# Performance work log

Measured on AMD Instinct MI355X. Metric: run time of the kernel, lower is better.

Reference implementation:

```python
import jax, jax.numpy as jnp
import numpy as np

NUM_ITER = 3  # self.num_iter


def setup_inputs() -> dict:
    key = jax.random.key(0)
    k1, k2, k3 = jax.random.split(key, 3)
    B, N, D = 8, 8192, 512          # batch, num_particles, dimension
    P, G, GS = 4, 512, 16           # num projs, groups per proj, group size
    x = jax.random.normal(k1, (B, N, D), dtype=jnp.float32)
    # per-proj feature projection (stand-in for proj.get_delta_x); small scale for stability
    W = jax.random.normal(k2, (P, D, D), dtype=jnp.float32) * 0.02
    groups = jax.random.randint(k3, (P, G, GS), 0, N, dtype=jnp.int32)
    return {"x": x, "W": W, "groups": groups}


def reference(x, W, groups):
    # x: [B, N, D]; W: [P, D, D]; groups: [P, G, GS] indices into N
    B, N, D = x.shape
    P = W.shape[0]
    upd = x
    for ite in range(NUM_ITER):
        scale = 1.0 / (ite + 1)  # ite-dependence of get_delta_x
        delta = jnp.zeros_like(upd)
        for i in range(P):
            g = groups[i]                      # [G, GS]
            gx = upd[:, g, :]                  # gather -> [B, G, GS, D]
            dx = scale * jnp.einsum('bgsd,de->bgse', gx, W[i])
            # scatter-add deltas back onto particle axis (overlaps accumulate)
            delta = delta.at[:, g.reshape(-1), :].add(dx.reshape(B, -1, D))
        upd = upd + delta
    return upd
```

## Files before the change

kernel.cpp:

```cpp
#include <hip/hip_runtime.h>
#include <stdint.h>

#define NROW 8192
#define DDIM 512
#define BB   8
#define PP   4
#define MTOT (BB*NROW)

typedef __attribute__((ext_vector_type(8))) short short8;
typedef __attribute__((ext_vector_type(4))) float floatx4;
typedef __attribute__((ext_vector_type(4))) unsigned int uintx4;

__device__ inline float bf2f(unsigned short h) { return __uint_as_float(((unsigned)h) << 16); }
__device__ inline unsigned short f2bf_rn(float f) {
    return (unsigned short)((__float_as_uint(f) + 0x8000u) >> 16);
}
__device__ inline unsigned pack_bf16(float a, float b) {
    unsigned ua = __float_as_uint(a) + 0x8000u;
    unsigned ub = __float_as_uint(b) + 0x8000u;
    return __builtin_amdgcn_perm(ub, ua, 0x07060302u);
}

template <typename T> __device__ inline float loadF(const T* p);
template <> __device__ inline float loadF<float>(const float* p) { return *p; }
template <> __device__ inline float loadF<unsigned short>(const unsigned short* p) { return bf2f(*p); }
template <typename T> __device__ inline void storeF(T* p, float f);
template <> __device__ inline void storeF<float>(float* p, float f) { *p = f; }
template <> __device__ inline void storeF<unsigned short>(unsigned short* p, float f) { *p = f2bf_rn(f); }

__global__ void hist_kernel(const int* __restrict__ groups, float* __restrict__ cnt) {
    int t = blockIdx.x * 256 + threadIdx.x;
    int i = t >> 13;
    atomicAdd(&cnt[i * NROW + groups[t]], 1.0f);
}

__global__ void transpose_w(const float* __restrict__ W, unsigned short* __restrict__ Wsw) {
    int u = blockIdx.x * 256 + threadIdx.x;
    int i    = u >> 15;
    int kb   = (u >> 11) & 15;
    int gt   = (u >> 6) & 31;
    int lane = u & 63;
    int n  = gt * 16 + (lane & 15);
    int k0 = kb * 32 + (lane >> 4) * 8;
    const float* wp = W + i * 262144 + k0 * 512 + n;
    unsigned hp[4];
    #pragma unroll
    for (int j = 0; j < 4; ++j)
        hp[j] = pack_bf16(wp[(2*j) * 512], wp[(2*j+1) * 512]);
    uintx4 w = {hp[0], hp[1], hp[2], hp[3]};
    *(uintx4*)(Wsw + (size_t)u * 8) = w;
}

template <typename SrcT, typename DstT>
__global__ __launch_bounds__(256, 2)
void gemm_round(const SrcT* __restrict__ src, const unsigned short* __restrict__ Wsw,
                const float* __restrict__ cnt, DstT* __restrict__ dst, float scale)
{
    __shared__ __align__(16) unsigned short sA[2][2048];
    __shared__ __align__(16) float sE[PP][16][64];

    const int t    = threadIdx.x;
    const int wave = t >> 6;
    const int lane = t & 63;
    const int m0   = blockIdx.x * 64;
    const int nb   = blockIdx.y;

    float cs[4][4];
    #pragma unroll
    for (int a = 0; a < 4; ++a)
        #pragma unroll
        for (int q = 0; q < 4; ++q)
            cs[a][q] = cnt[wave * NROW + ((m0 + a*16 + (lane >> 4)*4 + q) & (NROW - 1))];

    const int srow = ((t >> 6) << 4) | (t & 15);
    const int scol = ((t >> 4) & 3) * 8;
    const SrcT* sp = src + (size_t)(m0 + srow) * DDIM + scol;
    unsigned short* sAw0 = &sA[0][t * 8];
    unsigned short* sAw1 = &sA[1][t * 8];

    const unsigned short* bp = Wsw + ((size_t)(wave * 16) * 32 + nb * 4) * 512 + lane * 8;

    floatx4 acc[4][4] = {};
    short8 Bc[2][4];

    #pragma unroll
    for (int b = 0; b < 4; ++b)
        Bc[0][b] = *(const short8*)(bp + b * 512);
    if constexpr (sizeof(SrcT) == 4) {
        floatx4 v0 = *(const floatx4*)(sp);
        floatx4 v1 = *(const floatx4*)(sp + 4);
        uintx4 w = { pack_bf16(v0[0], v0[1]), pack_bf16(v0[2], v0[3]),
                     pack_bf16(v1[0], v1[1]), pack_bf16(v1[2], v1[3]) };
        *(uintx4*)sAw0 = w;
    } else {
        *(uintx4*)sAw0 = *(const uintx4*)sp;
    }
    __syncthreads();

    #pragma unroll
    for (int kb = 0; kb < 16; ++kb) {
        const int cur = kb & 1;
        unsigned short* sAwn = cur ? sAw0 : sAw1;

        floatx4 v0, v1; uintx4 vr;
        if (kb < 15) {
            if constexpr (sizeof(SrcT) == 4) {
                v0 = *(const floatx4*)(sp + (kb + 1) * 32);
                v1 = *(const floatx4*)(sp + (kb + 1) * 32 + 4);
            } else {
                vr = *(const uintx4*)(sp + (kb + 1) * 32);
            }
            #pragma unroll
            for (int b = 0; b < 4; ++b)
                Bc[cur ^ 1][b] = *(const short8*)(bp + (size_t)(kb + 1) * 16384 + b * 512);
        }

        short8 af[4];
        #pragma unroll
        for (int a = 0; a < 4; ++a)
            af[a] = *(const short8*)&sA[cur][(a * 64 + lane) * 8];

        #pragma unroll
        for (int a = 0; a < 4; ++a)
            #pragma unroll
            for (int b = 0; b < 4; ++b)
                acc[a][b] = __builtin_amdgcn_mfma_f32_16x16x32_bf16(af[a], Bc[cur][b], acc[a][b], 0, 0, 0);

        if (kb < 15) {
            if constexpr (sizeof(SrcT) == 4) {
                uintx4 w = { pack_bf16(v0[0], v0[1]), pack_bf16(v0[2], v0[3]),
                             pack_bf16(v1[0], v1[1]), pack_bf16(v1[2], v1[3]) };
                *(uintx4*)sAwn = w;
            } else {
                *(uintx4*)sAwn = vr;
            }
        }
        __syncthreads();
    }

    #pragma unroll
    for (int a = 0; a < 4; ++a) {
        #pragma unroll
        for (int b = 0; b < 4; ++b)
            #pragma unroll
            for (int q = 0; q < 4; ++q)
                sE[wave][(lane >> 4) * 4 + q][b * 16 + (lane & 15)] = acc[a][b][q] * cs[a][q];
        __syncthreads();
        #pragma unroll
        for (int e = 0; e < 4; ++e) {
            const int r = wave * 4 + e;
            const size_t m = (size_t)(m0 + a * 16 + r);
            const size_t n = (size_t)nb * 64 + lane;
            const float sum = sE[0][r][lane] + sE[1][r][lane] + sE[2][r][lane] + sE[3][r][lane];
            storeF(dst + m * DDIM + n, loadF(src + m * DDIM + n) + scale * sum);
        }
        if (a < 3) __syncthreads();
    }
}

extern "C" void kernel_launch(void* const* d_in, const int* in_sizes, int n_in,
                              void* d_out, int out_size, void* d_ws, size_t ws_size,
                              hipStream_t stream) {
    const float* x      = (const float*)d_in[0];
    const float* W      = (const float*)d_in[1];
    const int*   groups = (const int*)d_in[2];
    float* out = (float*)d_out;

    char* ws = (char*)d_ws;
    float*          cnt = (float*)ws;
    unsigned short* Wsw = (unsigned short*)(ws + 131072);
    unsigned short* U   = (unsigned short*)(ws + 131072 + 2097152);

    hipMemsetAsync(cnt, 0, PP * NROW * sizeof(float), stream);
    hist_kernel<<<32768 / 256, 256, 0, stream>>>(groups, cnt);
    transpose_w<<<131072 / 256, 256, 0, stream>>>(W, Wsw);

    dim3 grid(MTOT / 64, DDIM / 64);
    gemm_round<float, float><<<grid, 256, 0, stream>>>(x, Wsw, cnt, out, 1.0f);
    gemm_round<float, unsigned short><<<grid, 256, 0, stream>>>(out, Wsw, cnt, U, 0.5f);
    gemm_round<unsigned short, float><<<grid, 256, 0, stream>>>(U, Wsw, cnt, out, 1.0f / 3.0f);
}
```

Before: 862.8 us.

## Deepen GEMM pipeline with two-stage k-steps, swap grid order, pad epilogue LDS

Restructures the gemm_round main loop to process two k-blocks per barrier, using a register prefetch two stages ahead and a lighter LDS-only barrier. This halves the number of block syncs. The grid is transposed so the N-blocks sharing one 64-row M-tile are launched together, which should improve L2 reuse of the source rows. It also aliases the epilogue buffer onto the A-tile shared memory and pads its rows to 65 to avoid bank conflicts. The cost is higher register pressure from the prefetch buffers, and relying on a custom barrier that only waits on lgkmcnt.

```diff
diff --git a/kernel.cpp b/kernel.cpp
--- a/kernel.cpp
+++ b/kernel.cpp
@@ -19,6 +19,11 @@
     unsigned ua = __float_as_uint(a) + 0x8000u;
     unsigned ub = __float_as_uint(b) + 0x8000u;
     return __builtin_amdgcn_perm(ub, ua, 0x07060302u);
+}
+__device__ inline uintx4 packA(const floatx4& v0, const floatx4& v1) {
+    uintx4 w = { pack_bf16(v0[0], v0[1]), pack_bf16(v0[2], v0[3]),
+                 pack_bf16(v1[0], v1[1]), pack_bf16(v1[2], v1[3]) };
+    return w;
 }
 
 template <typename T> __device__ inline float loadF(const T* p);
@@ -27,6 +32,13 @@
 template <typename T> __device__ inline void storeF(T* p, float f);
 template <> __device__ inline void storeF<float>(float* p, float f) { *p = f; }
 template <> __device__ inline void storeF<unsigned short>(unsigned short* p, float f) { *p = f2bf_rn(f); }
+
+__device__ inline void block_sync_lds() {
+    __builtin_amdgcn_sched_barrier(0);
+    asm volatile("s_waitcnt lgkmcnt(0)" ::: "memory");
+    __builtin_amdgcn_s_barrier();
+    __builtin_amdgcn_sched_barrier(0);
+}
 
 __global__ void hist_kernel(const int* __restrict__ groups, float* __restrict__ cnt) {
     int t = blockIdx.x * 256 + threadIdx.x;
@@ -56,102 +68,139 @@
 void gemm_round(const SrcT* __restrict__ src, const unsigned short* __restrict__ Wsw,
                 const float* __restrict__ cnt, DstT* __restrict__ dst, float scale)
 {
-    __shared__ __align__(16) unsigned short sA[2][2048];
-    __shared__ __align__(16) float sE[PP][16][64];
+    __shared__ __align__(16) unsigned char smem[16768];
+    unsigned short* sA = (unsigned short*)smem;
+    float*          sE = (float*)smem;
 
     const int t    = threadIdx.x;
     const int wave = t >> 6;
     const int lane = t & 63;
-    const int m0   = blockIdx.x * 64;
-    const int nb   = blockIdx.y;
-
-    float cs[4][4];
-    #pragma unroll
-    for (int a = 0; a < 4; ++a)
-        #pragma unroll
-        for (int q = 0; q < 4; ++q)
-            cs[a][q] = cnt[wave * NROW + ((m0 + a*16 + (lane >> 4)*4 + q) & (NROW - 1))];
+    const int nb   = blockIdx.x;
+    const int m0   = blockIdx.y * 64;
 
     const int srow = ((t >> 6) << 4) | (t & 15);
     const int scol = ((t >> 4) & 3) * 8;
     const SrcT* sp = src + (size_t)(m0 + srow) * DDIM + scol;
-    unsigned short* sAw0 = &sA[0][t * 8];
-    unsigned short* sAw1 = &sA[1][t * 8];
+    unsigned short* sAw = sA + t * 8;
 
     const unsigned short* bp = Wsw + ((size_t)(wave * 16) * 32 + nb * 4) * 512 + lane * 8;
 
     floatx4 acc[4][4] = {};
-    short8 Bc[2][4];
-
+    short8 Bf[2][4];
+    floatx4 pf[2][2];
+    uintx4  pb[2];
+
+    #pragma unroll
+    for (int s = 0; s < 2; ++s) {
+        if constexpr (sizeof(SrcT) == 4) {
+            floatx4 v0 = *(const floatx4*)(sp + s * 32);
+            floatx4 v1 = *(const floatx4*)(sp + s * 32 + 4);
+            *(uintx4*)(sAw + s * 2048) = packA(v0, v1);
+        } else {
+            *(uintx4*)(sAw + s * 2048) = *(const uintx4*)(sp + s * 32);
+        }
+    }
+    #pragma unroll
+    for (int s = 0; s < 2; ++s) {
+        if constexpr (sizeof(SrcT) == 4) {
+            pf[s][0] = *(const floatx4*)(sp + (2 + s) * 32);
+            pf[s][1] = *(const floatx4*)(sp + (2 + s) * 32 + 4);
+        } else {
+            pb[s] = *(const uintx4*)(sp + (2 + s) * 32);
+        }
+    }
     #pragma unroll
     for (int b = 0; b < 4; ++b)
-        Bc[0][b] = *(const short8*)(bp + b * 512);
-    if constexpr (sizeof(SrcT) == 4) {
-        floatx4 v0 = *(const floatx4*)(sp);
-        floatx4 v1 = *(const floatx4*)(sp + 4);
-        uintx4 w = { pack_bf16(v0[0], v0[1]), pack_bf16(v0[2], v0[3]),
-                     pack_bf16(v1[0], v1[1]), pack_bf16(v1[2], v1[3]) };
-        *(uintx4*)sAw0 = w;
-    } else {
-        *(uintx4*)sAw0 = *(const uintx4*)sp;
-    }
-    __syncthreads();
-
-    #pragma unroll
-    for (int kb = 0; kb < 16; ++kb) {
-        const int cur = kb & 1;
-        unsigned short* sAwn = cur ? sAw0 : sAw1;
-
-        floatx4 v0, v1; uintx4 vr;
-        if (kb < 15) {
-            if constexpr (sizeof(SrcT) == 4) {
-                v0 = *(const floatx4*)(sp + (kb + 1) * 32);
-                v1 = *(const floatx4*)(sp + (kb + 1) * 32 + 4);
-            } else {
-                vr = *(const uintx4*)(sp + (kb + 1) * 32);
+        Bf[0][b] = *(const short8*)(bp + b * 512);
+    block_sync_lds();
+
+    #pragma unroll
+    for (int it = 0; it < 8; ++it) {
+        const int buf = it & 1;
+        const unsigned short* sAr = sA + buf * 4096;
+
+        #pragma unroll
+        for (int b = 0; b < 4; ++b)
+            Bf[1][b] = *(const short8*)(bp + (size_t)(2 * it + 1) * 16384 + b * 512);
+
+        {
+            short8 af[4];
+            #pragma unroll
+            for (int a = 0; a < 4; ++a)
+                af[a] = *(const short8*)(sAr + (a * 64 + lane) * 8);
+            #pragma unroll
+            for (int a = 0; a < 4; ++a)
+                #pragma unroll
+                for (int b = 0; b < 4; ++b)
+                    acc[a][b] = __builtin_amdgcn_mfma_f32_16x16x32_bf16(af[a], Bf[0][b], acc[a][b], 0, 0, 0);
+        }
+
+        if (it < 7) {
+            #pragma unroll
+            for (int b = 0; b < 4; ++b)
+                Bf[0][b] = *(const short8*)(bp + (size_t)(2 * it + 2) * 16384 + b * 512);
+        }
+
+        {
+            short8 af[4];
+            #pragma unroll
+            for (int a = 0; a < 4; ++a)
+                af[a] = *(const short8*)(sAr + 2048 + (a * 64 + lane) * 8);
+            #pragma unroll
+            for (int a = 0; a < 4; ++a)
+                #pragma unroll
+                for (int b = 0; b < 4; ++b)
+                    acc[a][b] = __builtin_amdgcn_mfma_f32_16x16x32_bf16(af[a], Bf[1][b], acc[a][b], 0, 0, 0);
+        }
+
+        if (it < 7) {
+            unsigned short* sAn = sA + (buf ^ 1) * 4096 + t * 8;
+            #pragma unroll
+            for (int s = 0; s < 2; ++s) {
+                if constexpr (sizeof(SrcT) == 4)
+                    *(uintx4*)(sAn + s * 2048) = packA(pf[s][0], pf[s][1]);
+                else
+                    *(uintx4*)(sAn + s * 2048) = pb[s];
             }
-            #pragma unroll
-            for (int b = 0; b < 4; ++b)
-                Bc[cur ^ 1][b] = *(const short8*)(bp + (size_t)(kb + 1) * 16384 + b * 512);
-        }
-
-        short8 af[4];
-        #pragma unroll
-        for (int a = 0; a < 4; ++a)
-            af[a] = *(const short8*)&sA[cur][(a * 64 + lane) * 8];
-
-        #pragma unroll
-        for (int a = 0; a < 4; ++a)
-            #pragma unroll
-            for (int b = 0; b < 4; ++b)
-                acc[a][b] = __builtin_amdgcn_mfma_f32_16x16x32_bf16(af[a], Bc[cur][b], acc[a][b], 0, 0, 0);
-
-        if (kb < 15) {
-            if constexpr (sizeof(SrcT) == 4) {
-                uintx4 w = { pack_bf16(v0[0], v0[1]), pack_bf16(v0[2], v0[3]),
-                             pack_bf16(v1[0], v1[1]), pack_bf16(v1[2], v1[3]) };
-                *(uintx4*)sAwn = w;
-            } else {
-                *(uintx4*)sAwn = vr;
+            if (it < 6) {
+                #pragma unroll
+                for (int s = 0; s < 2; ++s) {
+                    const int c = (2 * (it + 2) + s) * 32;
+                    if constexpr (sizeof(SrcT) == 4) {
+                        pf[s][0] = *(const floatx4*)(sp + c);
+                        pf[s][1] = *(const floatx4*)(sp + c + 4);
+                    } else {
+                        pb[s] = *(const uintx4*)(sp + c);
+                    }
+                }
             }
         }
-        __syncthreads();
-    }
+        block_sync_lds();
+    }
+
+    float cs[4][4];
+    #pragma unroll
+    for (int a = 0; a < 4; ++a)
+        #pragma unroll
+        for (int q = 0; q < 4; ++q)
+            cs[a][q] = cnt[wave * NROW + ((m0 + a * 16 + (lane >> 4) * 4 + q) & (NROW - 1))];
 
     #pragma unroll
     for (int a = 0; a < 4; ++a) {
+        float* se = sE + wave * 1040;
         #pragma unroll
         for (int b = 0; b < 4; ++b)
             #pragma unroll
             for (int q = 0; q < 4; ++q)
-                sE[wave][(lane >> 4) * 4 + q][b * 16 + (lane & 15)] = acc[a][b][q] * cs[a][q];
+                se[((lane >> 4) * 4 + q) * 65 + b * 16 + (lane & 15)] = acc[a][b][q] * cs[a][q];
         __syncthreads();
         #pragma unroll
         for (int e = 0; e < 4; ++e) {
             const int r = wave * 4 + e;
             const size_t m = (size_t)(m0 + a * 16 + r);
             const size_t n = (size_t)nb * 64 + lane;
-            const float sum = sE[0][r][lane] + sE[1][r][lane] + sE[2][r][lane] + sE[3][r][lane];
+            const float sum = sE[0 * 1040 + r * 65 + lane] + sE[1 * 1040 + r * 65 + lane]
+                            + sE[2 * 1040 + r * 65 + lane] + sE[3 * 1040 + r * 65 + lane];
             storeF(dst + m * DDIM + n, loadF(src + m * DDIM + n) + scale * sum);
         }
         if (a < 3) __syncthreads();
@@ -175,7 +224,7 @@
     hist_kernel<<<32768 / 256, 256, 0, stream>>>(groups, cnt);
     transpose_w<<<131072 / 256, 256, 0, stream>>>(W, Wsw);
 
-    dim3 grid(MTOT / 64, DDIM / 64);
+    dim3 grid(DDIM / 64, MTOT / 64);
     gemm_round<float, float><<<grid, 256, 0, stream>>>(x, Wsw, cnt, out, 1.0f);
     gemm_round<float, unsigned short><<<grid, 256, 0, stream>>>(out, Wsw, cnt, U, 0.5f);
     gemm_round<unsigned short, float><<<grid, 256, 0, stream>>>(U, Wsw, cnt, out, 1.0f / 3.0f);
```

Measured after the change: 776.1 us. 1.11x faster.

## Stage bf16 A tiles via global_load_lds with triple-buffered pipeline

Applied to the files above, without the earlier changes.

Inputs are now converted to bf16 up front in a separate kernel. Each round writes a bf16 copy of its output alongside (or instead of) fp32, so every GEMM reads the A operand as bf16. A tiles are loaded straight into LDS with global_load_lds in a three-buffer ring paced by explicit vmcnt waits. W fragments are prefetched four slots deep in registers. The grid is reordered so consecutive blocks share an M tile across N blocks, and the epilogue LDS is padded to avoid bank conflicts. The aim is to remove the register-staged conversion and the per-k-step full barriers, at the cost of an extra conversion pass and more writes of bf16 intermediates.

```diff
diff --git a/kernel.cpp b/kernel.cpp
--- a/kernel.cpp
+++ b/kernel.cpp
@@ -20,13 +20,28 @@
     unsigned ub = __float_as_uint(b) + 0x8000u;
     return __builtin_amdgcn_perm(ub, ua, 0x07060302u);
 }
+__device__ inline uintx4 packA(const floatx4& v0, const floatx4& v1) {
+    uintx4 w = { pack_bf16(v0[0], v0[1]), pack_bf16(v0[2], v0[3]),
+                 pack_bf16(v1[0], v1[1]), pack_bf16(v1[2], v1[3]) };
+    return w;
+}
 
 template <typename T> __device__ inline float loadF(const T* p);
 template <> __device__ inline float loadF<float>(const float* p) { return *p; }
 template <> __device__ inline float loadF<unsigned short>(const unsigned short* p) { return bf2f(*p); }
-template <typename T> __device__ inline void storeF(T* p, float f);
-template <> __device__ inline void storeF<float>(float* p, float f) { *p = f; }
-template <> __device__ inline void storeF<unsigned short>(unsigned short* p, float f) { *p = f2bf_rn(f); }
+
+__device__ inline void glds16(const void* g, void* l) {
+    __builtin_amdgcn_global_load_lds(
+        (const __attribute__((address_space(1))) void*)g,
+        (__attribute__((address_space(3))) void*)l, 16, 0, 0);
+}
+
+#define SYNC_VM(N) do {                                                 \
+    __builtin_amdgcn_sched_barrier(0);                                  \
+    asm volatile("s_waitcnt vmcnt(" #N ") lgkmcnt(0)" ::: "memory");    \
+    __builtin_amdgcn_s_barrier();                                       \
+    __builtin_amdgcn_sched_barrier(0);                                  \
+} while (0)
 
 __global__ void hist_kernel(const int* __restrict__ groups, float* __restrict__ cnt) {
     int t = blockIdx.x * 256 + threadIdx.x;
@@ -51,108 +66,116 @@
     *(uintx4*)(Wsw + (size_t)u * 8) = w;
 }
 
-template <typename SrcT, typename DstT>
+__global__ void cvt_bf16(const float* __restrict__ x, unsigned short* __restrict__ xb) {
+    size_t t = (size_t)blockIdx.x * 256 + threadIdx.x;
+    const floatx4* p = (const floatx4*)x + t * 2;
+    floatx4 v0 = p[0], v1 = p[1];
+    *(uintx4*)(xb + t * 8) = packA(v0, v1);
+}
+
+template <typename AddT, bool WF32, bool WBF16>
 __global__ __launch_bounds__(256, 2)
-void gemm_round(const SrcT* __restrict__ src, const unsigned short* __restrict__ Wsw,
-                const float* __restrict__ cnt, DstT* __restrict__ dst, float scale)
+void gemm_round(const unsigned short* __restrict__ srcA, const AddT* __restrict__ srcAdd,
+                const unsigned short* __restrict__ Wsw, const float* __restrict__ cnt,
+                float* __restrict__ dstF, unsigned short* __restrict__ dstB, float scale)
 {
-    __shared__ __align__(16) unsigned short sA[2][2048];
-    __shared__ __align__(16) float sE[PP][16][64];
+    __shared__ __align__(16) unsigned char smem[24576];
+    float* sE = (float*)smem;
 
     const int t    = threadIdx.x;
     const int wave = t >> 6;
     const int lane = t & 63;
-    const int m0   = blockIdx.x * 64;
-    const int nb   = blockIdx.y;
+    const int nb   = blockIdx.x;
+    const int m0   = blockIdx.y * 64;
+
+    const int srow = (wave << 4) | (lane & 15);
+    const int scol = ((lane >> 4) & 3) * 8;
+    const unsigned short* sp = srcA + (size_t)(m0 + srow) * DDIM + scol;
+
+    const unsigned short* bp = Wsw + ((size_t)(wave * 16) * 32 + nb * 4) * 512 + lane * 8;
+
+    floatx4 acc[4][4] = {};
+    short8 Bf[4][4];
+
+    auto stage = [&](int buf, int it2) {
+        #pragma unroll
+        for (int s = 0; s < 2; ++s)
+            glds16(sp + (2 * it2 + s) * 32, smem + (buf * 2 + s) * 4096 + wave * 1024);
+    };
+    auto loadB = [&](int slot, int s) {
+        #pragma unroll
+        for (int b = 0; b < 4; ++b)
+            Bf[slot][b] = *(const short8*)(bp + (size_t)s * 16384 + b * 512);
+    };
+
+    stage(0, 0);
+    stage(1, 1);
+    __builtin_amdgcn_sched_barrier(0);
+    loadB(0, 0); loadB(1, 1); loadB(2, 2);
+    SYNC_VM(14);
+
+    #pragma unroll
+    for (int it = 0; it < 8; ++it) {
+        const unsigned short* sAr = (const unsigned short*)(smem + (it % 3) * 8192);
+
+        short8 af[2][4];
+        #pragma unroll
+        for (int s = 0; s < 2; ++s)
+            #pragma unroll
+            for (int a = 0; a < 4; ++a)
+                af[s][a] = *(const short8*)(sAr + s * 2048 + (a * 64 + lane) * 8);
+
+        if (it < 6) stage((it + 2) % 3, it + 2);
+        __builtin_amdgcn_sched_barrier(0);
+        if (it < 7) loadB((2 * it + 3) & 3, 2 * it + 3);
+        __builtin_amdgcn_sched_barrier(0);
+
+        #pragma unroll
+        for (int a = 0; a < 4; ++a)
+            #pragma unroll
+            for (int b = 0; b < 4; ++b)
+                acc[a][b] = __builtin_amdgcn_mfma_f32_16x16x32_bf16(af[0][a], Bf[(2 * it) & 3][b], acc[a][b], 0, 0, 0);
+
+        if (it < 6) loadB((2 * it + 4) & 3, 2 * it + 4);
+        __builtin_amdgcn_sched_barrier(0);
+
+        #pragma unroll
+        for (int a = 0; a < 4; ++a)
+            #pragma unroll
+            for (int b = 0; b < 4; ++b)
+                acc[a][b] = __builtin_amdgcn_mfma_f32_16x16x32_bf16(af[1][a], Bf[(2 * it + 1) & 3][b], acc[a][b], 0, 0, 0);
+
+        if (it < 6)       SYNC_VM(10);
+        else if (it == 6) SYNC_VM(4);
+        else              SYNC_VM(0);
+    }
 
     float cs[4][4];
     #pragma unroll
     for (int a = 0; a < 4; ++a)
         #pragma unroll
         for (int q = 0; q < 4; ++q)
-            cs[a][q] = cnt[wave * NROW + ((m0 + a*16 + (lane >> 4)*4 + q) & (NROW - 1))];
-
-    const int srow = ((t >> 6) << 4) | (t & 15);
-    const int scol = ((t >> 4) & 3) * 8;
-    const SrcT* sp = src + (size_t)(m0 + srow) * DDIM + scol;
-    unsigned short* sAw0 = &sA[0][t * 8];
-    unsigned short* sAw1 = &sA[1][t * 8];
-
-    const unsigned short* bp = Wsw + ((size_t)(wave * 16) * 32 + nb * 4) * 512 + lane * 8;
-
-    floatx4 acc[4][4] = {};
-    short8 Bc[2][4];
-
-    #pragma unroll
-    for (int b = 0; b < 4; ++b)
-        Bc[0][b] = *(const short8*)(bp + b * 512);
-    if constexpr (sizeof(SrcT) == 4) {
-        floatx4 v0 = *(const floatx4*)(sp);
-        floatx4 v1 = *(const floatx4*)(sp + 4);
-        uintx4 w = { pack_bf16(v0[0], v0[1]), pack_bf16(v0[2], v0[3]),
-                     pack_bf16(v1[0], v1[1]), pack_bf16(v1[2], v1[3]) };
-        *(uintx4*)sAw0 = w;
-    } else {
-        *(uintx4*)sAw0 = *(const uintx4*)sp;
-    }
-    __syncthreads();
-
-    #pragma unroll
-    for (int kb = 0; kb < 16; ++kb) {
-        const int cur = kb & 1;
-        unsigned short* sAwn = cur ? sAw0 : sAw1;
-
-        floatx4 v0, v1; uintx4 vr;
-        if (kb < 15) {
-            if constexpr (sizeof(SrcT) == 4) {
-                v0 = *(const floatx4*)(sp + (kb + 1) * 32);
-                v1 = *(const floatx4*)(sp + (kb + 1) * 32 + 4);
-            } else {
-                vr = *(const uintx4*)(sp + (kb + 1) * 32);
-            }
-            #pragma unroll
-            for (int b = 0; b < 4; ++b)
-                Bc[cur ^ 1][b] = *(const short8*)(bp + (size_t)(kb + 1) * 16384 + b * 512);
-        }
-
-        short8 af[4];
-        #pragma unroll
-        for (int a = 0; a < 4; ++a)
-            af[a] = *(const short8*)&sA[cur][(a * 64 + lane) * 8];
-
-        #pragma unroll
-        for (int a = 0; a < 4; ++a)
-            #pragma unroll
-            for (int b = 0; b < 4; ++b)
-                acc[a][b] = __builtin_amdgcn_mfma_f32_16x16x32_bf16(af[a], Bc[cur][b], acc[a][b], 0, 0, 0);
-
-        if (kb < 15) {
-            if constexpr (sizeof(SrcT) == 4) {
-                uintx4 w = { pack_bf16(v0[0], v0[1]), pack_bf16(v0[2], v0[3]),
-                             pack_bf16(v1[0], v1[1]), pack_bf16(v1[2], v1[3]) };
-                *(uintx4*)sAwn = w;
-            } else {
-                *(uintx4*)sAwn = vr;
-            }
-        }
-        __syncthreads();
-    }
+            cs[a][q] = cnt[wave * NROW + ((m0 + a * 16 + (lane >> 4) * 4 + q) & (NROW - 1))];
 
     #pragma unroll
     for (int a = 0; a < 4; ++a) {
+        float* se = sE + wave * 1104;
         #pragma unroll
         for (int b = 0; b < 4; ++b)
             #pragma unroll
             for (int q = 0; q < 4; ++q)
-                sE[wave][(lane >> 4) * 4 + q][b * 16 + (lane & 15)] = acc[a][b][q] * cs[a][q];
+                se[((lane >> 4) * 4 + q) * 69 + b * 16 + (lane & 15)] = acc[a][b][q] * cs[a][q];
         __syncthreads();
         #pragma unroll
         for (int e = 0; e < 4; ++e) {
             const int r = wave * 4 + e;
             const size_t m = (size_t)(m0 + a * 16 + r);
             const size_t n = (size_t)nb * 64 + lane;
-            const float sum = sE[0][r][lane] + sE[1][r][lane] + sE[2][r][lane] + sE[3][r][lane];
-            storeF(dst + m * DDIM + n, loadF(src + m * DDIM + n) + scale * sum);
+            const float sum = sE[0 * 1104 + r * 69 + lane] + sE[1 * 1104 + r * 69 + lane]
+                            + sE[2 * 1104 + r * 69 + lane] + sE[3 * 1104 + r * 69 + lane];
+            const float f = loadF(srcAdd + m * DDIM + n) + scale * sum;
+            if constexpr (WF32)  dstF[m * DDIM + n] = f;
+            if constexpr (WBF16) dstB[m * DDIM + n] = f2bf_rn(f);
         }
         if (a < 3) __syncthreads();
     }
@@ -169,14 +192,16 @@
     char* ws = (char*)d_ws;
     float*          cnt = (float*)ws;
     unsigned short* Wsw = (unsigned short*)(ws + 131072);
-    unsigned short* U   = (unsigned short*)(ws + 131072 + 2097152);
+    unsigned short* U1  = (unsigned short*)(ws + 131072 + 2097152);
+    unsigned short* U2  = U1 + (size_t)MTOT * DDIM;
 
     hipMemsetAsync(cnt, 0, PP * NROW * sizeof(float), stream);
     hist_kernel<<<32768 / 256, 256, 0, stream>>>(groups, cnt);
     transpose_w<<<131072 / 256, 256, 0, stream>>>(W, Wsw);
-
-    dim3 grid(MTOT / 64, DDIM / 64);
-    gemm_round<float, float><<<grid, 256, 0, stream>>>(x, Wsw, cnt, out, 1.0f);
-    gemm_round<float, unsigned short><<<grid, 256, 0, stream>>>(out, Wsw, cnt, U, 0.5f);
-    gemm_round<unsigned short, float><<<grid, 256, 0, stream>>>(U, Wsw, cnt, out, 1.0f / 3.0f);
-}
+    cvt_bf16<<<(MTOT * DDIM / 8) / 256, 256, 0, stream>>>(x, U2);
+
+    dim3 grid(DDIM / 64, MTOT / 64);
+    gemm_round<float, true, true><<<grid, 256, 0, stream>>>(U2, x, Wsw, cnt, out, U1, 1.0f);
+    gemm_round<float, false, true><<<grid, 256, 0, stream>>>(U1, out, Wsw, cnt, nullptr, U2, 0.5f);
+    gemm_round<unsigned short, true, false><<<grid, 256, 0, stream>>>(U2, U2, Wsw, cnt, out, nullptr, 1.0f / 3.0f);
+}
```

After: 832.7 us. -3.5%, faster.
